# Kernel optimization log

Hardware: AMD Instinct MI355X
Metric: run time of the kernel (lower is better)

Reference implementation:

```python
import jax, jax.numpy as jnp
import numpy as np

N_NODES = 100000
E2 = 1600000
E3 = 1600000
ES = 100000
HID = 64


def _mlp_3x3(x_in, W1, b1, W2, b2):
    # x_in: [E, d_in] -> mobility [E, 3, 3]
    h = jax.nn.relu(x_in @ W1 + b1)
    out = h @ W2 + b2  # [E, 9]
    return out.reshape(-1, 3, 3)


def setup_inputs() -> dict:
    key = jax.random.key(0)
    ks = jax.random.split(key, 20)
    inp = {}
    inp["x"] = jax.random.normal(ks[0], (N_NODES, 3), dtype=jnp.float32)
    inp["edge_2body"] = jax.random.randint(ks[1], (2, E2), 0, N_NODES)
    inp["edge_3body"] = jax.random.randint(ks[2], (3, E3), 0, N_NODES)
    inp["edge_2bodySelf"] = jax.random.randint(ks[3], (2, ES), 0, N_NODES)
    inp["edge_1body"] = jax.random.randint(ks[4], (2, ES), 0, N_NODES)
    inp["edge_attr_2body"] = jax.random.normal(ks[5], (E2, 3), dtype=jnp.float32)
    inp["edge_attr_3body"] = jax.random.normal(ks[6], (E3, 3), dtype=jnp.float32)
    inp["edge_attr_2bodySelf"] = jax.random.normal(ks[7], (ES, 3), dtype=jnp.float32)
    inp["edge_attr_1body"] = jax.random.normal(ks[8], (ES, 3), dtype=jnp.float32)
    s = 0.1
    # nn_2body: 3 -> HID -> 9
    inp["W1_2b"] = jax.random.normal(ks[9], (3, HID), dtype=jnp.float32) * s
    inp["b1_2b"] = jnp.zeros((HID,), jnp.float32)
    inp["W2_2b"] = jax.random.normal(ks[10], (HID, 9), dtype=jnp.float32) * s
    inp["b2_2b"] = jnp.zeros((9,), jnp.float32)
    # nn_3body: 6 -> HID -> 9
    inp["W1_3b"] = jax.random.normal(ks[11], (6, HID), dtype=jnp.float32) * s
    inp["b1_3b"] = jnp.zeros((HID,), jnp.float32)
    inp["W2_3b"] = jax.random.normal(ks[12], (HID, 9), dtype=jnp.float32) * s
    inp["b2_3b"] = jnp.zeros((9,), jnp.float32)
    # nn_self: 3 -> HID -> 9
    inp["W1_s"] = jax.random.normal(ks[13], (3, HID), dtype=jnp.float32) * s
    inp["b1_s"] = jnp.zeros((HID,), jnp.float32)
    inp["W2_s"] = jax.random.normal(ks[14], (HID, 9), dtype=jnp.float32) * s
    inp["b2_s"] = jnp.zeros((9,), jnp.float32)
    return inp


def reference(x, edge_2body, edge_3body, edge_2bodySelf, edge_1body,
              edge_attr_2body, edge_attr_3body, edge_attr_2bodySelf, edge_attr_1body,
              W1_2b, b1_2b, W2_2b, b2_2b,
              W1_3b, b1_3b, W2_3b, b2_3b,
              W1_s, b1_s, W2_s, b2_s):
    n = x.shape[0]
    # ---- 2-body: gather -> MLP -> per-edge 3x3 matvec -> scatter-add ----
    d2 = x[edge_2body[0]] - x[edge_2body[1]]  # xj - xi, [E2,3]
    mob2 = _mlp_3x3(d2, W1_2b, b1_2b, W2_2b, b2_2b)
    y2 = jnp.einsum('eij,ej->ei', mob2, edge_attr_2body)
    v2 = jax.ops.segment_sum(y2, edge_2body[1], num_segments=n)
    # ---- 3-body ----
    xj = x[edge_3body[0]]
    xk = x[edge_3body[1]]
    xi = x[edge_3body[2]]
    d3 = jnp.concatenate((xk - xj, xi - xk), axis=1)  # [E3,6]
    mob3 = _mlp_3x3(d3, W1_3b, b1_3b, W2_3b, b2_3b)
    y3 = jnp.einsum('eij,ej->ei', mob3, edge_attr_3body)
    v3 = jax.ops.segment_sum(y3, edge_3body[2], num_segments=n)
    # ---- 2-body self ----
    ds = x[edge_2bodySelf[0]] - x[edge_2bodySelf[1]]
    mobs = _mlp_3x3(ds, W1_s, b1_s, W2_s, b2_s)
    ys = jnp.einsum('eij,ej->ei', mobs, edge_attr_2bodySelf)
    vs = jax.ops.segment_sum(ys, edge_2bodySelf[1], num_segments=n)
    # edge_1body / edge_attr_1body unused in original forward
    return v2 + v3 + vs
```

## Files before the change

### kernel.cpp

```cpp
#include <hip/hip_runtime.h>


constexpr int HIDDEN = 64;
constexpr int NB_MAX = 256;
constexpr int NPB_SHIFT = 9;
constexpr int NPB = 1 << NPB_SHIFT;
constexpr int SSPLIT = 4;
constexpr int TILE_F = NPB * 3;
constexpr int TILE_F4 = TILE_F / 4;

template <int DIN>
__global__ __launch_bounds__(1024) void p1_edge_kernel(
    const float* __restrict__ x,
    const int* __restrict__ edges, long long E,
    const float* __restrict__ attr,
    const float* __restrict__ W1, const float* __restrict__ b1,
    const float* __restrict__ W2, const float* __restrict__ b2,
    float4* __restrict__ records, int* __restrict__ gcount, int cap)
{
    constexpr int BLK = 1024;
    constexpr int KPT = 2;

    __shared__ int s_hist[NB_MAX];
    __shared__ int s_base[NB_MAX];
    __shared__ int s_rank[NB_MAX];

    const int tid = threadIdx.x;
    const long long span = (E + gridDim.x - 1) / gridDim.x;
    const long long lo = (long long)blockIdx.x * span;
    const long long hi = (lo + span < E) ? (lo + span) : E;

    for (int i = tid; i < NB_MAX; i += BLK) { s_hist[i] = 0; s_rank[i] = 0; }
    __syncthreads();

    const long long dstrow = (DIN == 3) ? E : 2 * E;
    for (long long e = lo + tid; e < hi; e += BLK) {
        int d = edges[dstrow + e];
        atomicAdd(&s_hist[d >> NPB_SHIFT], 1);
    }
    __syncthreads();

    for (int i = tid; i < NB_MAX; i += BLK) {
        int h = s_hist[i];
        s_base[i] = (h > 0) ? atomicAdd(&gcount[i], h) : 0;
    }
    __syncthreads();

    for (long long t0 = lo; t0 < hi; t0 += BLK * KPT) {
        float d[KPT][DIN];
        float a[KPT][3];
        int   dst[KPT];
        bool  valid[KPT];

        #pragma unroll
        for (int u = 0; u < KPT; ++u) {
            long long e = t0 + (long long)u * BLK + tid;
            valid[u] = (e < hi);
            long long ee = valid[u] ? e : lo;
            if constexpr (DIN == 3) {
                int s = edges[ee];
                int t = edges[E + ee];
                dst[u] = t;
                #pragma unroll
                for (int c = 0; c < 3; ++c)
                    d[u][c] = x[3 * (long long)s + c] - x[3 * (long long)t + c];
            } else {
                int j = edges[ee];
                int k = edges[E + ee];
                int i = edges[2 * E + ee];
                dst[u] = i;
                #pragma unroll
                for (int c = 0; c < 3; ++c) {
                    float xj = x[3 * (long long)j + c];
                    float xk = x[3 * (long long)k + c];
                    float xi = x[3 * (long long)i + c];
                    d[u][c]     = xk - xj;
                    d[u][3 + c] = xi - xk;
                }
            }
            #pragma unroll
            for (int c = 0; c < 3; ++c) a[u][c] = attr[3 * ee + c];
        }

        float acc[KPT][9];
        #pragma unroll
        for (int u = 0; u < KPT; ++u)
            #pragma unroll
            for (int i = 0; i < 9; ++i) acc[u][i] = b2[i];

        #pragma unroll 4
        for (int hh = 0; hh < HIDDEN; ++hh) {
            const float bb = b1[hh];
            float w1r[DIN];
            #pragma unroll
            for (int r = 0; r < DIN; ++r) w1r[r] = W1[r * HIDDEN + hh];
            float w2r[9];
            #pragma unroll
            for (int i = 0; i < 9; ++i) w2r[i] = W2[hh * 9 + i];
            #pragma unroll
            for (int u = 0; u < KPT; ++u) {
                float pre = bb;
                #pragma unroll
                for (int r = 0; r < DIN; ++r) pre = fmaf(d[u][r], w1r[r], pre);
                const float h = fmaxf(pre, 0.0f);
                #pragma unroll
                for (int i = 0; i < 9; ++i) acc[u][i] = fmaf(h, w2r[i], acc[u][i]);
            }
        }

        #pragma unroll
        for (int u = 0; u < KPT; ++u) {
            if (!valid[u]) continue;
            float y0 = fmaf(acc[u][0], a[u][0], fmaf(acc[u][1], a[u][1], acc[u][2] * a[u][2]));
            float y1 = fmaf(acc[u][3], a[u][0], fmaf(acc[u][4], a[u][1], acc[u][5] * a[u][2]));
            float y2 = fmaf(acc[u][6], a[u][0], fmaf(acc[u][7], a[u][1], acc[u][8] * a[u][2]));
            int b = dst[u] >> NPB_SHIFT;
            int r = atomicAdd(&s_rank[b], 1);
            int slot = s_base[b] + r;
            if (slot < cap)
                records[(size_t)b * cap + slot] =
                    make_float4(y0, y1, y2, __int_as_float(dst[u]));
        }
    }
}

__global__ __launch_bounds__(256) void p2_partial(
    const float4* __restrict__ records, const int* __restrict__ gcount,
    int cap, float* __restrict__ partials)
{
    __shared__ float s_acc[TILE_F];
    const int b = blockIdx.x / SSPLIT;
    const int s = blockIdx.x % SSPLIT;
    const int tid = threadIdx.x;

    for (int i = tid; i < TILE_F; i += 256) s_acc[i] = 0.0f;
    __syncthreads();

    int cnt = gcount[b];
    if (cnt > cap) cnt = cap;
    const int chunk = (cnt + SSPLIT - 1) / SSPLIT;
    const int beg = s * chunk;
    const int end = min(beg + chunk, cnt);

    const float4* rb = records + (size_t)b * cap;
    for (int i = beg + tid; i < end; i += 256) {
        float4 r = rb[i];
        int loc = __float_as_int(r.w) - (b << NPB_SHIFT);
        atomicAdd(&s_acc[loc * 3 + 0], r.x);
        atomicAdd(&s_acc[loc * 3 + 1], r.y);
        atomicAdd(&s_acc[loc * 3 + 2], r.z);
    }
    __syncthreads();

    float* pt = partials + (size_t)blockIdx.x * TILE_F;
    for (int i = tid; i < TILE_F; i += 256) pt[i] = s_acc[i];
}

__global__ __launch_bounds__(256) void p2_final(
    const float4* __restrict__ partials, float4* __restrict__ out, int n4)
{
    int i4 = blockIdx.x * 256 + threadIdx.x;
    if (i4 >= n4) return;
    int b = i4 / TILE_F4;
    int loc = i4 - b * TILE_F4;
    const float4* base = partials + (size_t)b * SSPLIT * TILE_F4 + loc;
    float4 sum = base[0];
    #pragma unroll
    for (int s = 1; s < SSPLIT; ++s) {
        float4 v = base[(size_t)s * TILE_F4];
        sum.x += v.x; sum.y += v.y; sum.z += v.z; sum.w += v.w;
    }
    out[i4] = sum;
}

__global__ void p2_final_tail(const float* __restrict__ partials,
                              float* __restrict__ out, int start, int n)
{
    int idx = start + blockIdx.x * 64 + threadIdx.x;
    if (idx >= n) return;
    int b = idx / TILE_F;
    int loc = idx - b * TILE_F;
    const float* base = partials + (size_t)b * SSPLIT * TILE_F + loc;
    float sum = 0.f;
    #pragma unroll
    for (int s = 0; s < SSPLIT; ++s) sum += base[(size_t)s * TILE_F];
    out[idx] = sum;
}

__global__ __launch_bounds__(256) void p2_reduce(
    const float4* __restrict__ records, const int* __restrict__ gcount,
    int cap, int n_nodes, float* __restrict__ out)
{
    __shared__ float s_acc[TILE_F];
    const int b = blockIdx.x;
    const int tid = threadIdx.x;
    for (int i = tid; i < TILE_F; i += 256) s_acc[i] = 0.0f;
    __syncthreads();
    int cnt = gcount[b];
    if (cnt > cap) cnt = cap;
    const float4* rb = records + (size_t)b * cap;
    for (int i = tid; i < cnt; i += 256) {
        float4 r = rb[i];
        int loc = __float_as_int(r.w) - (b << NPB_SHIFT);
        atomicAdd(&s_acc[loc * 3 + 0], r.x);
        atomicAdd(&s_acc[loc * 3 + 1], r.y);
        atomicAdd(&s_acc[loc * 3 + 2], r.z);
    }
    __syncthreads();
    const int start = (b << NPB_SHIFT) * 3;
    const int end = min(n_nodes * 3, ((b + 1) << NPB_SHIFT) * 3);
    for (int i = start + tid; i < end; i += 256)
        out[i] = s_acc[i - start];
}

template <int DIN, int KPT>
__global__ __launch_bounds__(256) void edge_mlp_atomic(
    const float* __restrict__ x,
    const int* __restrict__ edges, long long E,
    const float* __restrict__ attr,
    const float* __restrict__ W1, const float* __restrict__ b1,
    const float* __restrict__ W2, const float* __restrict__ b2,
    float* __restrict__ out)
{
    const int tid = threadIdx.x;
    const long long base = (long long)blockIdx.x * (blockDim.x * KPT) + tid;
    float d[KPT][DIN]; float a[KPT][3]; int dst[KPT]; bool valid[KPT];
    #pragma unroll
    for (int u = 0; u < KPT; ++u) {
        long long e = base + (long long)u * blockDim.x;
        valid[u] = (e < E);
        long long ee = valid[u] ? e : 0;
        if constexpr (DIN == 3) {
            int s = edges[ee]; int t = edges[E + ee]; dst[u] = t;
            #pragma unroll
            for (int c = 0; c < 3; ++c)
                d[u][c] = x[3 * (long long)s + c] - x[3 * (long long)t + c];
        } else {
            int j = edges[ee]; int k = edges[E + ee]; int i = edges[2 * E + ee];
            dst[u] = i;
            #pragma unroll
            for (int c = 0; c < 3; ++c) {
                float xj = x[3 * (long long)j + c];
                float xk = x[3 * (long long)k + c];
                float xi = x[3 * (long long)i + c];
                d[u][c] = xk - xj; d[u][3 + c] = xi - xk;
            }
        }
        #pragma unroll
        for (int c = 0; c < 3; ++c) a[u][c] = attr[3 * ee + c];
    }
    float acc[KPT][9];
    #pragma unroll
    for (int u = 0; u < KPT; ++u)
        #pragma unroll
        for (int i = 0; i < 9; ++i) acc[u][i] = b2[i];
    #pragma unroll 4
    for (int hh = 0; hh < HIDDEN; ++hh) {
        const float bb = b1[hh];
        float w1r[DIN];
        #pragma unroll
        for (int r = 0; r < DIN; ++r) w1r[r] = W1[r * HIDDEN + hh];
        float w2r[9];
        #pragma unroll
        for (int i = 0; i < 9; ++i) w2r[i] = W2[hh * 9 + i];
        #pragma unroll
        for (int u = 0; u < KPT; ++u) {
            float pre = bb;
            #pragma unroll
            for (int r = 0; r < DIN; ++r) pre = fmaf(d[u][r], w1r[r], pre);
            const float h = fmaxf(pre, 0.0f);
            #pragma unroll
            for (int i = 0; i < 9; ++i) acc[u][i] = fmaf(h, w2r[i], acc[u][i]);
        }
    }
    #pragma unroll
    for (int u = 0; u < KPT; ++u) {
        if (!valid[u]) continue;
        float* o = out + 3 * (long long)dst[u];
        #pragma unroll
        for (int i = 0; i < 3; ++i) {
            float y = fmaf(acc[u][3 * i + 0], a[u][0],
                      fmaf(acc[u][3 * i + 1], a[u][1],
                           acc[u][3 * i + 2] * a[u][2]));
            atomicAdd(&o[i], y);
        }
    }
}

extern "C" void kernel_launch(void* const* d_in, const int* in_sizes, int n_in,
                              void* d_out, int out_size, void* d_ws, size_t ws_size,
                              hipStream_t stream)
{
    const float* x  = (const float*)d_in[0];
    const int*   e2 = (const int*)d_in[1];
    const int*   e3 = (const int*)d_in[2];
    const int*   es = (const int*)d_in[3];
    const float* a2 = (const float*)d_in[5];
    const float* a3 = (const float*)d_in[6];
    const float* as = (const float*)d_in[7];
    const float* W1_2b = (const float*)d_in[9];
    const float* b1_2b = (const float*)d_in[10];
    const float* W2_2b = (const float*)d_in[11];
    const float* b2_2b = (const float*)d_in[12];
    const float* W1_3b = (const float*)d_in[13];
    const float* b1_3b = (const float*)d_in[14];
    const float* W2_3b = (const float*)d_in[15];
    const float* b2_3b = (const float*)d_in[16];
    const float* W1_s  = (const float*)d_in[17];
    const float* b1_s  = (const float*)d_in[18];
    const float* W2_s  = (const float*)d_in[19];
    const float* b2_s  = (const float*)d_in[20];

    const long long E2 = in_sizes[1] / 2;
    const long long E3 = in_sizes[2] / 3;
    const long long ES = in_sizes[3] / 2;
    const long long Etot = E2 + E3 + ES;
    const int n_nodes = out_size / 3;
    const int nbuckets = (n_nodes + NPB - 1) >> NPB_SHIFT;

    float* out = (float*)d_out;

    const size_t off_part = 4096;
    const size_t part_bytes = (size_t)nbuckets * SSPLIT * TILE_F * sizeof(float);
    long long mean_per_bucket = (Etot + nbuckets - 1) / nbuckets;
    long long min_cap = mean_per_bucket + 1600;

    constexpr int P1_BLK = 1024, P1_KPT = 2;
    const long long p1_tile = (long long)P1_BLK * P1_KPT;
    int g2 = (int)((E2 + p1_tile - 1) / p1_tile);
    int g3 = (int)((E3 + p1_tile - 1) / p1_tile);
    int gs = (int)((ES + p1_tile - 1) / p1_tile);

    long long cap_avail_split =
        ((long long)ws_size - (long long)off_part - (long long)part_bytes) /
        ((long long)nbuckets * 16);
    long long cap_avail_plain =
        ((long long)ws_size - (long long)off_part) / ((long long)nbuckets * 16);

    if (nbuckets <= NB_MAX && cap_avail_split >= min_cap) {
        long long capL = min_cap + 4096;
        if (capL > cap_avail_split) capL = cap_avail_split;
        int cap = (int)capL;
        int* gcount = (int*)d_ws;
        float* partials = (float*)((char*)d_ws + off_part);
        float4* records = (float4*)((char*)d_ws + off_part + part_bytes);

        hipMemsetAsync(gcount, 0, NB_MAX * sizeof(int), stream);

        if (g2 > 0)
            p1_edge_kernel<3><<<g2, P1_BLK, 0, stream>>>(
                x, e2, E2, a2, W1_2b, b1_2b, W2_2b, b2_2b, records, gcount, cap);
        if (g3 > 0)
            p1_edge_kernel<6><<<g3, P1_BLK, 0, stream>>>(
                x, e3, E3, a3, W1_3b, b1_3b, W2_3b, b2_3b, records, gcount, cap);
        if (gs > 0)
            p1_edge_kernel<3><<<gs, P1_BLK, 0, stream>>>(
                x, es, ES, as, W1_s, b1_s, W2_s, b2_s, records, gcount, cap);

        p2_partial<<<nbuckets * SSPLIT, 256, 0, stream>>>(records, gcount, cap, partials);

        int n4 = out_size / 4;
        int tail = out_size - n4 * 4;
        if (n4 > 0)
            p2_final<<<(n4 + 255) / 256, 256, 0, stream>>>(
                (const float4*)partials, (float4*)out, n4);
        if (tail > 0)
            p2_final_tail<<<1, 64, 0, stream>>>(partials, out, n4 * 4, out_size);
    } else if (nbuckets <= NB_MAX && cap_avail_plain >= min_cap) {
        long long capL = min_cap + 4096;
        if (capL > cap_avail_plain) capL = cap_avail_plain;
        int cap = (int)capL;
        int* gcount = (int*)d_ws;
        float4* records = (float4*)((char*)d_ws + off_part);

        hipMemsetAsync(gcount, 0, NB_MAX * sizeof(int), stream);

        if (g2 > 0)
            p1_edge_kernel<3><<<g2, P1_BLK, 0, stream>>>(
                x, e2, E2, a2, W1_2b, b1_2b, W2_2b, b2_2b, records, gcount, cap);
        if (g3 > 0)
            p1_edge_kernel<6><<<g3, P1_BLK, 0, stream>>>(
                x, e3, E3, a3, W1_3b, b1_3b, W2_3b, b2_3b, records, gcount, cap);
        if (gs > 0)
            p1_edge_kernel<3><<<gs, P1_BLK, 0, stream>>>(
                x, es, ES, as, W1_s, b1_s, W2_s, b2_s, records, gcount, cap);

        p2_reduce<<<nbuckets, 256, 0, stream>>>(records, gcount, cap, n_nodes, out);
    } else {
        hipMemsetAsync(out, 0, (size_t)out_size * sizeof(float), stream);
        constexpr int BLK = 256, KPT = 4;
        const long long per_blk = (long long)BLK * KPT;
        int a2g = (int)((E2 + per_blk - 1) / per_blk);
        int a3g = (int)((E3 + per_blk - 1) / per_blk);
        int asg = (int)((ES + per_blk - 1) / per_blk);
        if (a2g > 0)
            edge_mlp_atomic<3, KPT><<<a2g, BLK, 0, stream>>>(
                x, e2, E2, a2, W1_2b, b1_2b, W2_2b, b2_2b, out);
        if (a3g > 0)
            edge_mlp_atomic<6, KPT><<<a3g, BLK, 0, stream>>>(
                x, e3, E3, a3, W1_3b, b1_3b, W2_3b, b2_3b, out);
        if (asg > 0)
            edge_mlp_atomic<3, KPT><<<asg, BLK, 0, stream>>>(
                x, es, ES, as, W1_s, b1_s, W2_s, b2_s, out);
    }
}
```

Before: 350.3 us.

## Pad node coords to float4, merge 2-body/self launches, retune edge blocks

```diff
diff --git a/kernel.cpp b/kernel.cpp
--- a/kernel.cpp
+++ b/kernel.cpp
@@ -5,30 +5,58 @@
 constexpr int NB_MAX = 256;
 constexpr int NPB_SHIFT = 9;
 constexpr int NPB = 1 << NPB_SHIFT;
-constexpr int SSPLIT = 4;
+constexpr int SSPLIT = 8;
 constexpr int TILE_F = NPB * 3;
 constexpr int TILE_F4 = TILE_F / 4;
 
+__global__ __launch_bounds__(256) void pad_x_kernel(
+    const float* __restrict__ x, float4* __restrict__ x4, int n)
+{
+    int i = blockIdx.x * 256 + threadIdx.x;
+    if (i >= n) return;
+    x4[i] = make_float4(x[3 * i], x[3 * i + 1], x[3 * i + 2], 0.0f);
+}
+
 template <int DIN>
-__global__ __launch_bounds__(1024) void p1_edge_kernel(
-    const float* __restrict__ x,
-    const int* __restrict__ edges, long long E,
-    const float* __restrict__ attr,
-    const float* __restrict__ W1, const float* __restrict__ b1,
-    const float* __restrict__ W2, const float* __restrict__ b2,
+__global__ __launch_bounds__(256) void p1_edge_kernel(
+    const float4* __restrict__ x4,
+    const int* __restrict__ edgesA, long long EA,
+    const float* __restrict__ attrA,
+    const float* __restrict__ W1A, const float* __restrict__ b1A,
+    const float* __restrict__ W2A, const float* __restrict__ b2A,
+    int GA,
+    const int* __restrict__ edgesB, long long EB,
+    const float* __restrict__ attrB,
+    const float* __restrict__ W1B, const float* __restrict__ b1B,
+    const float* __restrict__ W2B, const float* __restrict__ b2B,
     float4* __restrict__ records, int* __restrict__ gcount, int cap)
 {
-    constexpr int BLK = 1024;
-    constexpr int KPT = 2;
+    constexpr int BLK = 256;
+    constexpr int KPT = 4;
 
     __shared__ int s_hist[NB_MAX];
     __shared__ int s_base[NB_MAX];
     __shared__ int s_rank[NB_MAX];
 
+    const int blk = blockIdx.x;
+    const int* edges; long long E; const float* attr;
+    const float* W1; const float* b1; const float* W2; const float* b2;
+    int bidx, nblk;
+    if (blk < GA) {
+        edges = edgesA; E = EA; attr = attrA;
+        W1 = W1A; b1 = b1A; W2 = W2A; b2 = b2A;
+        bidx = blk; nblk = GA;
+    } else {
+        edges = edgesB; E = EB; attr = attrB;
+        W1 = W1B; b1 = b1B; W2 = W2B; b2 = b2B;
+        bidx = blk - GA; nblk = gridDim.x - GA;
+    }
+
     const int tid = threadIdx.x;
-    const long long span = (E + gridDim.x - 1) / gridDim.x;
-    const long long lo = (long long)blockIdx.x * span;
+    const long long span = (E + nblk - 1) / nblk;
+    const long long lo = (long long)bidx * span;
     const long long hi = (lo + span < E) ? (lo + span) : E;
+    if (lo >= E) return;
 
     for (int i = tid; i < NB_MAX; i += BLK) { s_hist[i] = 0; s_rank[i] = 0; }
     __syncthreads();
@@ -61,22 +89,25 @@
                 int s = edges[ee];
                 int t = edges[E + ee];
                 dst[u] = t;
-                #pragma unroll
-                for (int c = 0; c < 3; ++c)
-                    d[u][c] = x[3 * (long long)s + c] - x[3 * (long long)t + c];
+                float4 xs = x4[s];
+                float4 xt = x4[t];
+                d[u][0] = xs.x - xt.x;
+                d[u][1] = xs.y - xt.y;
+                d[u][2] = xs.z - xt.z;
             } else {
                 int j = edges[ee];
                 int k = edges[E + ee];
                 int i = edges[2 * E + ee];
                 dst[u] = i;
-                #pragma unroll
-                for (int c = 0; c < 3; ++c) {
-                    float xj = x[3 * (long long)j + c];
-                    float xk = x[3 * (long long)k + c];
-                    float xi = x[3 * (long long)i + c];
-                    d[u][c]     = xk - xj;
-                    d[u][3 + c] = xi - xk;
-                }
+                float4 xj = x4[j];
+                float4 xk = x4[k];
+                float4 xi = x4[i];
+                d[u][0] = xk.x - xj.x;
+                d[u][1] = xk.y - xj.y;
+                d[u][2] = xk.z - xj.z;
+                d[u][3] = xi.x - xk.x;
+                d[u][4] = xi.y - xk.y;
+                d[u][5] = xi.z - xk.z;
             }
             #pragma unroll
             for (int c = 0; c < 3; ++c) a[u][c] = attr[3 * ee + c];
@@ -187,32 +218,6 @@
     out[idx] = sum;
 }
 
-__global__ __launch_bounds__(256) void p2_reduce(
-    const float4* __restrict__ records, const int* __restrict__ gcount,
-    int cap, int n_nodes, float* __restrict__ out)
-{
-    __shared__ float s_acc[TILE_F];
-    const int b = blockIdx.x;
-    const int tid = threadIdx.x;
-    for (int i = tid; i < TILE_F; i += 256) s_acc[i] = 0.0f;
-    __syncthreads();
-    int cnt = gcount[b];
-    if (cnt > cap) cnt = cap;
-    const float4* rb = records + (size_t)b * cap;
-    for (int i = tid; i < cnt; i += 256) {
-        float4 r = rb[i];
-        int loc = __float_as_int(r.w) - (b << NPB_SHIFT);
-        atomicAdd(&s_acc[loc * 3 + 0], r.x);
-        atomicAdd(&s_acc[loc * 3 + 1], r.y);
-        atomicAdd(&s_acc[loc * 3 + 2], r.z);
-    }
-    __syncthreads();
-    const int start = (b << NPB_SHIFT) * 3;
-    const int end = min(n_nodes * 3, ((b + 1) << NPB_SHIFT) * 3);
-    for (int i = start + tid; i < end; i += 256)
-        out[i] = s_acc[i - start];
-}
-
 template <int DIN, int KPT>
 __global__ __launch_bounds__(256) void edge_mlp_atomic(
     const float* __restrict__ x,
@@ -285,6 +290,13 @@
             atomicAdd(&o[i], y);
         }
     }
+}
+
+static inline int grid_for(long long E, int span_target) {
+    long long g = (E + span_target - 1) / span_target;
+    if (g < 1) g = 1;
+    if (g > 4096) g = 4096;
+    return (int)g;
 }
 
 extern "C" void kernel_launch(void* const* d_in, const int* in_sizes, int n_in,
@@ -320,42 +332,44 @@
 
     float* out = (float*)d_out;
 
-    const size_t off_part = 4096;
+    const size_t off_x4 = 4096;
+    const size_t x4_bytes = (size_t)n_nodes * sizeof(float4);
+    const size_t off_part = off_x4 + ((x4_bytes + 255) & ~(size_t)255);
     const size_t part_bytes = (size_t)nbuckets * SSPLIT * TILE_F * sizeof(float);
+    const size_t off_rec = off_part + part_bytes;
+
     long long mean_per_bucket = (Etot + nbuckets - 1) / nbuckets;
     long long min_cap = mean_per_bucket + 1600;
-
-    constexpr int P1_BLK = 1024, P1_KPT = 2;
-    const long long p1_tile = (long long)P1_BLK * P1_KPT;
-    int g2 = (int)((E2 + p1_tile - 1) / p1_tile);
-    int g3 = (int)((E3 + p1_tile - 1) / p1_tile);
-    int gs = (int)((ES + p1_tile - 1) / p1_tile);
-
-    long long cap_avail_split =
-        ((long long)ws_size - (long long)off_part - (long long)part_bytes) /
-        ((long long)nbuckets * 16);
-    long long cap_avail_plain =
-        ((long long)ws_size - (long long)off_part) / ((long long)nbuckets * 16);
-
-    if (nbuckets <= NB_MAX && cap_avail_split >= min_cap) {
+    long long cap_avail =
+        ((long long)ws_size - (long long)off_rec) / ((long long)nbuckets * 16);
+
+    constexpr int SPAN = 800;
+    int g2 = grid_for(E2, SPAN);
+    int g3 = grid_for(E3, SPAN);
+    int gs = grid_for(ES, SPAN);
+
+    if (nbuckets <= NB_MAX && cap_avail >= min_cap) {
         long long capL = min_cap + 4096;
-        if (capL > cap_avail_split) capL = cap_avail_split;
+        if (capL > cap_avail) capL = cap_avail;
         int cap = (int)capL;
         int* gcount = (int*)d_ws;
+        float4* x4 = (float4*)((char*)d_ws + off_x4);
         float* partials = (float*)((char*)d_ws + off_part);
-        float4* records = (float4*)((char*)d_ws + off_part + part_bytes);
+        float4* records = (float4*)((char*)d_ws + off_rec);
 
         hipMemsetAsync(gcount, 0, NB_MAX * sizeof(int), stream);
-
-        if (g2 > 0)
-            p1_edge_kernel<3><<<g2, P1_BLK, 0, stream>>>(
-                x, e2, E2, a2, W1_2b, b1_2b, W2_2b, b2_2b, records, gcount, cap);
-        if (g3 > 0)
-            p1_edge_kernel<6><<<g3, P1_BLK, 0, stream>>>(
-                x, e3, E3, a3, W1_3b, b1_3b, W2_3b, b2_3b, records, gcount, cap);
-        if (gs > 0)
-            p1_edge_kernel<3><<<gs, P1_BLK, 0, stream>>>(
-                x, es, ES, as, W1_s, b1_s, W2_s, b2_s, records, gcount, cap);
+        pad_x_kernel<<<(n_nodes + 255) / 256, 256, 0, stream>>>(x, x4, n_nodes);
+
+        p1_edge_kernel<3><<<g2 + gs, 256, 0, stream>>>(
+            x4,
+            e2, E2, a2, W1_2b, b1_2b, W2_2b, b2_2b, g2,
+            es, ES, as, W1_s, b1_s, W2_s, b2_s,
+            records, gcount, cap);
+        p1_edge_kernel<6><<<g3, 256, 0, stream>>>(
+            x4,
+            e3, E3, a3, W1_3b, b1_3b, W2_3b, b2_3b, g3,
+            nullptr, 0, nullptr, nullptr, nullptr, nullptr, nullptr,
+            records, gcount, cap);
 
         p2_partial<<<nbuckets * SSPLIT, 256, 0, stream>>>(records, gcount, cap, partials);
 
@@ -366,26 +380,6 @@
                 (const float4*)partials, (float4*)out, n4);
         if (tail > 0)
             p2_final_tail<<<1, 64, 0, stream>>>(partials, out, n4 * 4, out_size);
-    } else if (nbuckets <= NB_MAX && cap_avail_plain >= min_cap) {
-        long long capL = min_cap + 4096;
-        if (capL > cap_avail_plain) capL = cap_avail_plain;
-        int cap = (int)capL;
-        int* gcount = (int*)d_ws;
-        float4* records = (float4*)((char*)d_ws + off_part);
-
-        hipMemsetAsync(gcount, 0, NB_MAX * sizeof(int), stream);
-
-        if (g2 > 0)
-            p1_edge_kernel<3><<<g2, P1_BLK, 0, stream>>>(
-                x, e2, E2, a2, W1_2b, b1_2b, W2_2b, b2_2b, records, gcount, cap);
-        if (g3 > 0)
-            p1_edge_kernel<6><<<g3, P1_BLK, 0, stream>>>(
-                x, e3, E3, a3, W1_3b, b1_3b, W2_3b, b2_3b, records, gcount, cap);
-        if (gs > 0)
-            p1_edge_kernel<3><<<gs, P1_BLK, 0, stream>>>(
-                x, es, ES, as, W1_s, b1_s, W2_s, b2_s, records, gcount, cap);
-
-        p2_reduce<<<nbuckets, 256, 0, stream>>>(records, gcount, cap, n_nodes, out);
     } else {
         hipMemsetAsync(out, 0, (size_t)out_size * sizeof(float), stream);
         constexpr int BLK = 256, KPT = 4;
```

Result: no change. 354.8 us (+1.3%).
